# Kernel optimization log

Hardware: AMD Instinct MI355X
Metric: run time of the kernel (lower is better)

Reference implementation:

```python
import jax, jax.numpy as jnp
import numpy as np

D, H, K = 384, 6, 8
B, NQ, NK = 4, 2048, 2048
EPS = 1e-5


def _ln(x, s, b):
    m = jnp.mean(x, axis=-1, keepdims=True)
    v = jnp.mean((x - m) ** 2, axis=-1, keepdims=True)
    return (x - m) * jax.lax.rsqrt(v + EPS) * s + b


def _mha(q, k, v, Wo, bo):
    # q,k,v: [B, N, D]
    dh = D // H
    qh = q.reshape(q.shape[0], q.shape[1], H, dh).transpose(0, 2, 1, 3)
    kh = k.reshape(k.shape[0], k.shape[1], H, dh).transpose(0, 2, 1, 3)
    vh = v.reshape(v.shape[0], v.shape[1], H, dh).transpose(0, 2, 1, 3)
    scores = jnp.einsum('bhqd,bhkd->bhqk', qh, kh) / jnp.sqrt(jnp.asarray(dh, q.dtype))
    attn = jax.nn.softmax(scores, axis=-1)
    out = jnp.einsum('bhqk,bhkd->bhqd', attn, vh)
    out = out.transpose(0, 2, 1, 3).reshape(q.shape[0], q.shape[1], D)
    return out @ Wo + bo


def _knn_edge(q_coords, k_coords, q_feats, k_feats):
    # coords: [B, N, 3]; feats: [B, N, D]. EdgeConv-style feature:
    # concat(neighbor_feat - center_feat, center_feat) -> [B, Nq, K, 2D]
    d2 = (jnp.sum(q_coords ** 2, -1)[:, :, None]
          + jnp.sum(k_coords ** 2, -1)[:, None, :]
          - 2.0 * jnp.einsum('bqc,bkc->bqk', q_coords, k_coords))
    _, idx = jax.lax.top_k(-d2, K)  # [B, Nq, K] nearest neighbors in key set
    neigh = jax.vmap(lambda f, i: f[i])(k_feats, idx)  # [B, Nq, K, D]
    center = jnp.broadcast_to(q_feats[:, :, None, :], neigh.shape)
    return jnp.concatenate([neigh - center, center], axis=-1)


def setup_inputs() -> dict:
    key = jax.random.key(0)
    ks = jax.random.split(key, 24)
    s = 0.02
    return {
        'query_points': jax.random.normal(ks[0], (B, 3 + D, NQ), jnp.float32),
        'key_points': jax.random.normal(ks[1], (B, 3 + D, NK), jnp.float32),
        'ln_in_s': jnp.ones((D,), jnp.float32), 'ln_in_b': jnp.zeros((D,), jnp.float32),
        'qkv_W': jax.random.normal(ks[2], (D, 3 * D), jnp.float32) * s,
        'attn_out_W': jax.random.normal(ks[3], (D, D), jnp.float32) * s,
        'attn_out_b': jnp.zeros((D,), jnp.float32),
        'ff_W1': jax.random.normal(ks[4], (D, 2 * D), jnp.float32) * s,
        'ff_b1': jnp.zeros((2 * D,), jnp.float32),
        'ff_W2': jax.random.normal(ks[5], (2 * D, D), jnp.float32) * s,
        'ff_b2': jnp.zeros((D,), jnp.float32),
        'ffn_s': jnp.ones((D,), jnp.float32), 'ffn_b': jnp.zeros((D,), jnp.float32),
        'knn1_W': jax.random.normal(ks[6], (2 * D, D), jnp.float32) * s,
        'knn1_b': jnp.zeros((D,), jnp.float32),
        'knn2_W': jax.random.normal(ks[7], (2 * D, D), jnp.float32) * s,
        'knn2_b': jnp.zeros((D,), jnp.float32),
        'self_merge_W': jax.random.normal(ks[8], (2 * D, D), jnp.float32) * s,
        'self_merge_b': jnp.zeros((D,), jnp.float32),
        'cross_merge_W': jax.random.normal(ks[9], (2 * D, D), jnp.float32) * s,
        'cross_merge_b': jnp.zeros((D,), jnp.float32),
        'cnq_s': jnp.ones((D,), jnp.float32), 'cnq_b': jnp.zeros((D,), jnp.float32),
        'cnk_s': jnp.ones((D,), jnp.float32), 'cnk_b': jnp.zeros((D,), jnp.float32),
        'cq_W': jax.random.normal(ks[10], (D, D), jnp.float32) * s,
        'ck_W': jax.random.normal(ks[11], (D, D), jnp.float32) * s,
        'cv_W': jax.random.normal(ks[12], (D, D), jnp.float32) * s,
    }


def reference(query_points, key_points, ln_in_s, ln_in_b, qkv_W, attn_out_W,
              attn_out_b, ff_W1, ff_b1, ff_W2, ff_b2, ffn_s, ffn_b,
              knn1_W, knn1_b, knn2_W, knn2_b, self_merge_W, self_merge_b,
              cross_merge_W, cross_merge_b, cnq_s, cnq_b, cnk_s, cnk_b,
              cq_W, ck_W, cv_W):
    qp = jnp.transpose(query_points, (0, 2, 1))  # [B, Nq, 3+D]
    kp = jnp.transpose(key_points, (0, 2, 1))    # [B, Nk, 3+D]
    q_coords, q_feats = qp[..., :3], qp[..., 3:]
    k_coords, k_feats = kp[..., :3], kp[..., 3:]

    # --- self attention + self kNN geometry ---
    norm_f = _ln(q_feats, ln_in_s, ln_in_b)
    qkv = norm_f @ qkv_W
    q, k, v = jnp.split(qkv, 3, axis=-1)
    attn_f = _mha(q, k, v, attn_out_W, attn_out_b)

    edge = _knn_edge(q_coords, q_coords, norm_f, norm_f)          # [B,Nq,K,2D]
    geom = jax.nn.leaky_relu(edge @ knn1_W + knn1_b, 0.2)
    geom = jnp.max(geom, axis=2)                                   # [B,Nq,D]

    attn_f = jnp.concatenate([attn_f, geom], axis=-1) @ self_merge_W + self_merge_b
    q_feats = attn_f + q_feats

    # --- cross attention + cross kNN geometry ---
    nq = _ln(q_feats, cnq_s, cnq_b)
    nk = _ln(k_feats, cnk_s, cnk_b)
    cross_f = _mha(nq @ cq_W, nk @ ck_W, nk @ cv_W, attn_out_W, attn_out_b)

    cedge = _knn_edge(q_coords, k_coords, nq, nk)                  # [B,Nq,K,2D]
    cgeom = jax.nn.leaky_relu(cedge @ knn2_W + knn2_b, 0.2)
    cgeom = jnp.max(cgeom, axis=2)

    cross_f = jnp.concatenate([cross_f, cgeom], axis=-1) @ cross_merge_W + cross_merge_b
    q_feats = q_feats + cross_f

    # --- feed forward ---
    h = _ln(q_feats, ffn_s, ffn_b)
    q_feats = q_feats + (jax.nn.gelu(h @ ff_W1 + ff_b1) @ ff_W2 + ff_b2)

    out = jnp.concatenate([q_coords, q_feats], axis=-1)
    return jnp.transpose(out, (0, 2, 1))  # [B, 3+D, Nq]
```

## Files before the change

kernel.cpp:

```cpp
#include <hip/hip_runtime.h>
#include <cstdint>
#include <cstddef>

#define NB 4
#define NN 2048
#define DD 384
#define NH 6

typedef float f4 __attribute__((ext_vector_type(4)));
typedef float f32x4 __attribute__((ext_vector_type(4)));
typedef short bf16x8 __attribute__((ext_vector_type(8)));
typedef unsigned u32x2 __attribute__((ext_vector_type(2)));

__device__ __forceinline__ float gelu_t(float x) {
  float x3 = x*x*x;
  return 0.5f*x*(1.0f + tanhf(0.7978845608028654f*(x + 0.044715f*x3)));
}

__device__ __forceinline__ unsigned short f2b(float f) {
  unsigned u = __builtin_bit_cast(unsigned, f);
  u += 0x7fffu + ((u >> 16) & 1u);
  return (unsigned short)(u >> 16);
}

__device__ __forceinline__ float b2f(unsigned short u) {
  return __builtin_bit_cast(float, ((unsigned)u) << 16);
}

__device__ __forceinline__ unsigned cvtpk(float a, float b) {
  unsigned r;
  asm("v_cvt_pk_bf16_f32 %0, %1, %2" : "=v"(r) : "v"(a), "v"(b));
  return r;
}

typedef __attribute__((address_space(1))) const void gvoid_t;
typedef __attribute__((address_space(3))) void lvoid_t;
__device__ __forceinline__ void gl16(const void* g, void* l) {
  __builtin_amdgcn_global_load_lds((gvoid_t*)g, (lvoid_t*)l, 16, 0, 0);
}

__device__ __forceinline__ unsigned long long shfl_xor_u64(unsigned long long v, int m) {
  unsigned lo = (unsigned)v, hi = (unsigned)(v >> 32);
  lo = (unsigned)__shfl_xor((int)lo, m);
  hi = (unsigned)__shfl_xor((int)hi, m);
  return ((unsigned long long)hi << 32) | lo;
}

__global__ __launch_bounds__(256) void split_k(const float* __restrict__ pts,
                                               float* __restrict__ coords,
                                               float* __restrict__ feats) {
  __shared__ float t[32][33];
  int b = blockIdx.z;
  int c0 = blockIdx.x*32, n0 = blockIdx.y*32;
  int tx = threadIdx.x, ty = threadIdx.y;
#pragma unroll
  for (int i = 0; i < 4; ++i) {
    int c = c0 + ty + i*8;
    if (c < 387) t[ty+i*8][tx] = pts[((size_t)b*387 + c)*NN + n0 + tx];
  }
  __syncthreads();
#pragma unroll
  for (int i = 0; i < 4; ++i) {
    int n = n0 + ty + i*8;
    int c = c0 + tx;
    if (c < 387) {
      float v = t[tx][ty+i*8];
      if (c < 3) coords[((size_t)b*NN + n)*4 + c] = v;
      else       feats[((size_t)b*NN + n)*DD + (c-3)] = v;
    }
  }
}

__global__ __launch_bounds__(256) void kprep_k(float* __restrict__ c4) {
  int i = blockIdx.x*256 + threadIdx.x;
  f4 v = *(f4*)(c4 + (size_t)i*4);
  v[3] = v[0]*v[0] + v[1]*v[1] + v[2]*v[2];
  *(f4*)(c4 + (size_t)i*4) = v;
}

__global__ __launch_bounds__(256) void pack_k(const float* __restrict__ coords,
                                              const float* __restrict__ feats,
                                              float* __restrict__ out) {
  __shared__ float t[32][33];
  int b = blockIdx.z;
  int c0 = blockIdx.x*32, n0 = blockIdx.y*32;
  int tx = threadIdx.x, ty = threadIdx.y;
#pragma unroll
  for (int i = 0; i < 4; ++i) {
    int n = n0 + ty + i*8;
    int c = c0 + tx;
    if (c < 387) {
      float v = (c < 3) ? coords[((size_t)b*NN + n)*4 + c]
                        : feats[((size_t)b*NN + n)*DD + (c-3)];
      t[tx][ty+i*8] = v;
    }
  }
  __syncthreads();
#pragma unroll
  for (int i = 0; i < 4; ++i) {
    int c = c0 + ty + i*8;
    if (c < 387) out[((size_t)b*387 + c)*NN + n0 + tx] = t[ty+i*8][tx];
  }
}

__device__ __forceinline__ void ln_body(const float* __restrict__ x,
                                        const float* __restrict__ g,
                                        const float* __restrict__ bb,
                                        unsigned short* __restrict__ o,
                                        int row) {
  int lane = threadIdx.x & 63;
  const float* xr = x + (size_t)row*DD;
  float v[6]; float s = 0.f;
#pragma unroll
  for (int i = 0; i < 6; ++i) { v[i] = xr[lane + i*64]; s += v[i]; }
#pragma unroll
  for (int off = 1; off < 64; off <<= 1) s += __shfl_xor(s, off);
  float mean = s * (1.f/384.f);
  float s2 = 0.f;
#pragma unroll
  for (int i = 0; i < 6; ++i) { float d = v[i] - mean; s2 += d*d; }
#pragma unroll
  for (int off = 1; off < 64; off <<= 1) s2 += __shfl_xor(s2, off);
  float rs = rsqrtf(s2*(1.f/384.f) + 1e-5f);
  unsigned short* orow = o + (size_t)row*DD;
#pragma unroll
  for (int i = 0; i < 6; ++i) {
    int c = lane + i*64;
    orow[c] = f2b((v[i]-mean)*rs*g[c] + bb[c]);
  }
}

__global__ __launch_bounds__(256) void ln_k(const float* __restrict__ x,
                                            const float* __restrict__ g,
                                            const float* __restrict__ bb,
                                            unsigned short* __restrict__ o) {
  ln_body(x, g, bb, o, blockIdx.x*4 + (threadIdx.x >> 6));
}

__global__ __launch_bounds__(256) void ln2_k(const float* __restrict__ x1,
                                             const float* __restrict__ g1,
                                             const float* __restrict__ b1,
                                             unsigned short* __restrict__ o1,
                                             const float* __restrict__ x2,
                                             const float* __restrict__ g2,
                                             const float* __restrict__ b2,
                                             unsigned short* __restrict__ o2) {
  int row = blockIdx.x*4 + (threadIdx.x >> 6);
  if (blockIdx.y == 0) ln_body(x1, g1, b1, o1, row);
  else                 ln_body(x2, g2, b2, o2, row);
}

struct WSrcs { const float* p[13]; };

__global__ __launch_bounds__(256) void wtrans_k(WSrcs srcs, unsigned short* __restrict__ dst) {
  constexpr int KK[13]  = {384,384,384,384,768,384,384,384,384,384,768,384,768};
  constexpr int NW[13]  = {1152,384,384,384,384,384,384,384,384,384,384,768,384};
  constexpr int MD[13]  = {0,0,2,0,0,0,0,0,0,2,0,0,0};
  constexpr int OFF[13] = {0,442368,589824,737280,884736,1179648,1327104,1474560,
                           1622016,1769472,1916928,2211840,2506752};
  constexpr int PFX[14] = {0,432,576,720,864,1152,1296,1440,1584,1728,1872,2160,2448,2736};
  int bid = blockIdx.x;
  int e = 0;
  while (bid >= PFX[e+1]) ++e;
  int t = bid - PFX[e];
  int K = KK[e], N = NW[e];
  int ntiles = N >> 5;
  int kt = t / ntiles, nt = t - kt*ntiles;
  const float* src = srcs.p[e];
  __shared__ float T[32][33];
  int tx = threadIdx.x & 31, ty = threadIdx.x >> 5;
  int n = nt*32 + tx;
#pragma unroll
  for (int i = 0; i < 4; ++i) {
    int k = kt*32 + ty + i*8;
    float v = src[(size_t)k*N + n];
    if (MD[e] == 2) v = src[(size_t)(k+384)*N + n] - v;
    T[ty+i*8][tx] = v;
  }
  __syncthreads();
#pragma unroll
  for (int i = 0; i < 4; ++i) {
    int nn = nt*32 + ty + i*8;
    int kk = kt*32 + tx;
    dst[(size_t)OFF[e] + (size_t)nn*K + kk] = f2b(T[tx][ty+i*8]);
  }
}

template<int ACT, int ACC, int OB>
__global__ __launch_bounds__(256) void mgemm_k(const unsigned short* __restrict__ A, int lda,
                                               const unsigned short* __restrict__ Wt,
                                               const float* __restrict__ bias,
                                               void* __restrict__ Cv, int ldc, int cofs,
                                               int Kd) {
  __shared__ char lds[49152];
  int tid = threadIdx.x;
  int lane = tid & 63, w = tid >> 6, g = lane >> 4, c = lane & 15;
  int wr = w >> 1, wc = w & 1;
  int m0 = blockIdx.y*128, n0 = blockIdx.x*64;
  int lrow = lane >> 3;
  int cswz = ((lane & 7) ^ lrow)*8;

  f32x4 acc[4][2];
#pragma unroll
  for (int mt = 0; mt < 4; ++mt)
#pragma unroll
    for (int nt = 0; nt < 2; ++nt) acc[mt][nt] = 0.f;

  int KT = Kd >> 6;
  {
    char* As = lds; char* Bs = lds + 16384;
#pragma unroll
    for (int i = 0; i < 4; ++i) {
      int rb = i*32 + w*8;
      gl16(A + (size_t)(m0 + rb + lrow)*lda + cswz, As + rb*128);
    }
#pragma unroll
    for (int i = 0; i < 2; ++i) {
      int rb = i*32 + w*8;
      gl16(Wt + (size_t)(n0 + rb + lrow)*Kd + cswz, Bs + rb*128);
    }
  }
  __syncthreads();

  for (int kt = 0; kt < KT; ++kt) {
    char* Asc = lds + (kt & 1)*24576;
    char* Bsc = Asc + 16384;
    if (kt + 1 < KT) {
      char* Asn = lds + ((kt + 1) & 1)*24576;
      char* Bsn = Asn + 16384;
      int k0 = (kt + 1)*64;
#pragma unroll
      for (int i = 0; i < 4; ++i) {
        int rb = i*32 + w*8;
        gl16(A + (size_t)(m0 + rb + lrow)*lda + k0 + cswz, Asn + rb*128);
      }
#pragma unroll
      for (int i = 0; i < 2; ++i) {
        int rb = i*32 + w*8;
        gl16(Wt + (size_t)(n0 + rb + lrow)*Kd + k0 + cswz, Bsn + rb*128);
      }
    }
#pragma unroll
    for (int kb = 0; kb < 2; ++kb) {
      bf16x8 af[4], bfr[2];
#pragma unroll
      for (int mt = 0; mt < 4; ++mt) {
        int row = wr*64 + mt*16 + c;
        int ch = (kb*4 + g) ^ (row & 7);
        af[mt] = *(const bf16x8*)(Asc + row*128 + ch*16);
      }
#pragma unroll
      for (int nt = 0; nt < 2; ++nt) {
        int row = wc*32 + nt*16 + c;
        int ch = (kb*4 + g) ^ (row & 7);
        bfr[nt] = *(const bf16x8*)(Bsc + row*128 + ch*16);
      }
#pragma unroll
      for (int mt = 0; mt < 4; ++mt)
#pragma unroll
        for (int nt = 0; nt < 2; ++nt)
          acc[mt][nt] = __builtin_amdgcn_mfma_f32_16x16x32_bf16(af[mt], bfr[nt], acc[mt][nt], 0, 0, 0);
    }
    __syncthreads();
  }

#pragma unroll
  for (int mt = 0; mt < 4; ++mt) {
#pragma unroll
    for (int nt = 0; nt < 2; ++nt) {
      int coln = n0 + wc*32 + nt*16 + c;
      float bval = bias ? bias[coln] : 0.f;
#pragma unroll
      for (int r = 0; r < 4; ++r) {
        int m = m0 + wr*64 + mt*16 + 4*g + r;
        float t = acc[mt][nt][r] + bval;
        if (ACT == 1) t = gelu_t(t);
        if (OB) {
          ((unsigned short*)Cv)[(size_t)m*ldc + cofs + coln] = f2b(t);
        } else {
          float* cp = (float*)Cv + (size_t)m*ldc + cofs + coln;
          if (ACC) t += *cp;
          *cp = t;
        }
      }
    }
  }
}

struct FSegs {
  const unsigned short* A[5];
  unsigned short* out[5];
  int ldc[5];
  int cofs[5];
};

__global__ __launch_bounds__(256) void fgemm_k(FSegs fs, const unsigned short* __restrict__ Wt) {
  __shared__ char lds[49152];
  int tid = threadIdx.x;
  int lane = tid & 63, w = tid >> 6, g = lane >> 4, c = lane & 15;
  int wr = w >> 1, wc = w & 1;
  int m0 = blockIdx.y*128, n0 = blockIdx.x*64;
  int seg = n0 / 384;
  const unsigned short* A = fs.A[seg];
  int lrow = lane >> 3;
  int cswz = ((lane & 7) ^ lrow)*8;

  f32x4 acc[4][2];
#pragma unroll
  for (int mt = 0; mt < 4; ++mt)
#pragma unroll
    for (int nt = 0; nt < 2; ++nt) acc[mt][nt] = 0.f;

  {
    char* As = lds; char* Bs = lds + 16384;
#pragma unroll
    for (int i = 0; i < 4; ++i) {
      int rb = i*32 + w*8;
      gl16(A + (size_t)(m0 + rb + lrow)*384 + cswz, As + rb*128);
    }
#pragma unroll
    for (int i = 0; i < 2; ++i) {
      int rb = i*32 + w*8;
      gl16(Wt + (size_t)(n0 + rb + lrow)*384 + cswz, Bs + rb*128);
    }
  }
  __syncthreads();

  for (int kt = 0; kt < 6; ++kt) {
    char* Asc = lds + (kt & 1)*24576;
    char* Bsc = Asc + 16384;
    if (kt + 1 < 6) {
      char* Asn = lds + ((kt + 1) & 1)*24576;
      char* Bsn = Asn + 16384;
      int k0 = (kt + 1)*64;
#pragma unroll
      for (int i = 0; i < 4; ++i) {
        int rb = i*32 + w*8;
        gl16(A + (size_t)(m0 + rb + lrow)*384 + k0 + cswz, Asn + rb*128);
      }
#pragma unroll
      for (int i = 0; i < 2; ++i) {
        int rb = i*32 + w*8;
        gl16(Wt + (size_t)(n0 + rb + lrow)*384 + k0 + cswz, Bsn + rb*128);
      }
    }
#pragma unroll
    for (int kb = 0; kb < 2; ++kb) {
      bf16x8 af[4], bfr[2];
#pragma unroll
      for (int mt = 0; mt < 4; ++mt) {
        int row = wr*64 + mt*16 + c;
        int ch = (kb*4 + g) ^ (row & 7);
        af[mt] = *(const bf16x8*)(Asc + row*128 + ch*16);
      }
#pragma unroll
      for (int nt = 0; nt < 2; ++nt) {
        int row = wc*32 + nt*16 + c;
        int ch = (kb*4 + g) ^ (row & 7);
        bfr[nt] = *(const bf16x8*)(Bsc + row*128 + ch*16);
      }
#pragma unroll
      for (int mt = 0; mt < 4; ++mt)
#pragma unroll
        for (int nt = 0; nt < 2; ++nt)
          acc[mt][nt] = __builtin_amdgcn_mfma_f32_16x16x32_bf16(af[mt], bfr[nt], acc[mt][nt], 0, 0, 0);
    }
    __syncthreads();
  }

  if (seg == 2) {
    unsigned short* vtp = fs.out[2];
    int bb = m0 >> 11;
    int tokb = (m0 & 2047) + wr*64 + 4*g;
#pragma unroll
    for (int mt = 0; mt < 4; ++mt) {
#pragma unroll
      for (int nt = 0; nt < 2; ++nt) {
        int cseg = (n0 - 768) + wc*32 + nt*16 + c;
        int h = cseg >> 6, d = cseg & 63;
        u32x2 pv;
        pv[0] = cvtpk(acc[mt][nt][0], acc[mt][nt][1]);
        pv[1] = cvtpk(acc[mt][nt][2], acc[mt][nt][3]);
        *(u32x2*)(vtp + ((size_t)((bb*NH + h)*64 + d))*NN + tokb + mt*16) = pv;
      }
    }
    return;
  }

  unsigned short* outp = fs.out[seg];
  int ldcs = fs.ldc[seg];
  int cbase = fs.cofs[seg] + (n0 - seg*384);
#pragma unroll
  for (int mt = 0; mt < 4; ++mt) {
#pragma unroll
    for (int nt = 0; nt < 2; ++nt) {
      int coln = cbase + wc*32 + nt*16 + c;
#pragma unroll
      for (int r = 0; r < 4; ++r) {
        int m = m0 + wr*64 + mt*16 + 4*g + r;
        outp[(size_t)m*ldcs + coln] = f2b(acc[mt][nt][r]);
      }
    }
  }
}

__global__ __launch_bounds__(256) void flashm_k(const unsigned short* __restrict__ qkvb,
                                                const unsigned short* __restrict__ vt,
                                                unsigned short* __restrict__ o) {
  __shared__ char smem[40960];
  char* PT = smem + 32768;
  int bid = blockIdx.x;
  int s = (bid & 7)*96 + (bid >> 3);
  int qt = s & 31; int hb = s >> 5;
  int h = hb % NH, b = hb / NH;
  int q0 = qt*64;
  int tid = threadIdx.x;
  int w = tid >> 6, lane = tid & 63, g = lane >> 4, c = lane & 15;
  int lrow = lane >> 3;
  int gsw = ((lane & 7) ^ lrow)*8;

  const unsigned short* kbase = qkvb + (size_t)b*NN*1152 + 384 + h*64;
  const unsigned short* vbase = vt + ((size_t)(b*NH + h))*64*NN;

  bf16x8 qf[2];
  {
    const unsigned short* qrow = qkvb + ((size_t)(b*NN + q0 + w*16 + c))*1152 + h*64;
    qf[0] = *(const bf16x8*)(qrow + 8*g);
    qf[1] = *(const bf16x8*)(qrow + 32 + 8*g);
  }
  f32x4 oacc[4];
#pragma unroll
  for (int i = 0; i < 4; ++i) oacc[i] = 0.f;
  float lsum = 0.f;

#define FSTAGE(bf, ktb) { \
    char* KB = smem + (bf)*16384; char* VB = KB + 8192; \
    gl16(kbase + (size_t)((ktb) + w*16 + lrow)*1152 + gsw,     KB + (w*16)*128); \
    gl16(kbase + (size_t)((ktb) + w*16 + 8 + lrow)*1152 + gsw, KB + (w*16+8)*128); \
    gl16(vbase + (size_t)(w*16 + lrow)*NN + (ktb) + gsw,       VB + (w*16)*128); \
    gl16(vbase + (size_t)(w*16 + 8 + lrow)*NN + (ktb) + gsw,   VB + (w*16+8)*128); }

  FSTAGE(0, 0);
  __syncthreads();

  for (int kt = 0; kt < 32; ++kt) {
    if (kt + 1 < 32) FSTAGE((kt + 1) & 1, (kt + 1)*64);
    char* KTc = smem + (kt & 1)*16384;
    char* VTc = KTc + 8192;

    f32x4 sT[4];
#pragma unroll
    for (int nt = 0; nt < 4; ++nt) sT[nt] = 0.f;
#pragma unroll
    for (int nt = 0; nt < 4; ++nt) {
      int krow = nt*16 + c;
#pragma unroll
      for (int kb = 0; kb < 2; ++kb) {
        int ch = ((kb*4 + g) ^ (krow & 7))*16;
        bf16x8 kf_ = *(const bf16x8*)(KTc + krow*128 + ch);
        sT[nt] = __builtin_amdgcn_mfma_f32_16x16x32_bf16(kf_, qf[kb], sT[nt], 0, 0, 0);
      }
    }

    int prow = w*16 + c;
    int pswz = (c & 7) << 4;
#pragma unroll
    for (int nt = 0; nt < 4; ++nt) {
      float p0 = __builtin_amdgcn_exp2f(sT[nt][0] * 0.18033688011112042f);
      float p1 = __builtin_amdgcn_exp2f(sT[nt][1] * 0.18033688011112042f);
      float p2 = __builtin_amdgcn_exp2f(sT[nt][2] * 0.18033688011112042f);
      float p3 = __builtin_amdgcn_exp2f(sT[nt][3] * 0.18033688011112042f);
      lsum += (p0 + p1) + (p2 + p3);
      u32x2 pk;
      pk[0] = cvtpk(p0, p1);
      pk[1] = cvtpk(p2, p3);
      *(u32x2*)(PT + prow*128 + ((nt*32 + 8*g) ^ pswz)) = pk;
    }

    bf16x8 pb[2];
#pragma unroll
    for (int kb = 0; kb < 2; ++kb)
      pb[kb] = *(const bf16x8*)(PT + prow*128 + (((kb*4 + g) ^ (c & 7))*16));

#pragma unroll
    for (int dt = 0; dt < 4; ++dt) {
      int vrow = dt*16 + c;
#pragma unroll
      for (int kb = 0; kb < 2; ++kb) {
        int ch = ((kb*4 + g) ^ (vrow & 7))*16;
        bf16x8 vf = *(const bf16x8*)(VTc + vrow*128 + ch);
        oacc[dt] = __builtin_amdgcn_mfma_f32_16x16x32_bf16(vf, pb[kb], oacc[dt], 0, 0, 0);
      }
    }
    __syncthreads();
  }
#undef FSTAGE

  lsum += __shfl_xor(lsum, 16);
  lsum += __shfl_xor(lsum, 32);
  float inv = 1.f / lsum;
  size_t orow = ((size_t)b*NN + q0 + w*16 + c)*DD + h*64;
#pragma unroll
  for (int dt = 0; dt < 4; ++dt) {
    u32x2 ov;
    ov[0] = cvtpk(oacc[dt][0]*inv, oacc[dt][1]*inv);
    ov[1] = cvtpk(oacc[dt][2]*inv, oacc[dt][3]*inv);
    *(u32x2*)(o + orow + dt*16 + 4*g) = ov;
  }
}

#define CEX(a, b) { \
  unsigned long long lo_ = bd[a] < bd[b] ? bd[a] : bd[b]; \
  unsigned long long hi_ = bd[a] < bd[b] ? bd[b] : bd[a]; \
  bd[a] = lo_; bd[b] = hi_; }

__global__ __launch_bounds__(256) void knn2_k(const float* __restrict__ qc4,
                                              const float* __restrict__ kc4,
                                              int* __restrict__ idx1,
                                              int* __restrict__ idx2) {
  const float* kcs = blockIdx.y ? kc4 : qc4;
  int* idxo = blockIdx.y ? idx2 : idx1;
  int lane = threadIdx.x & 63;
  int q = blockIdx.x*4 + (threadIdx.x >> 6);
  int b = q >> 11;
  f4 qv = *(const f4*)(qc4 + (size_t)q*4);
  unsigned long long bd[8];
#pragma unroll
  for (int i = 0; i < 8; ++i) bd[i] = ~0ull;
  const float* kb = kcs + (size_t)b*NN*4;
#pragma unroll 4
  for (int j = lane; j < NN; j += 64) {
    f4 kv = *(const f4*)(kb + (size_t)j*4);
    float f = kv[3] - 2.f*(qv[0]*kv[0] + qv[1]*kv[1] + qv[2]*kv[2]);
    unsigned u = __builtin_bit_cast(unsigned, f);
    u ^= 0x80000000u | (unsigned)((int)u >> 31);
    unsigned long long key = ((unsigned long long)u << 32) | (unsigned)j;
#pragma unroll
    for (int k = 0; k < 8; ++k) {
      unsigned long long lo = key < bd[k] ? key : bd[k];
      unsigned long long hi = key < bd[k] ? bd[k] : key;
      bd[k] = lo; key = hi;
    }
  }
#pragma unroll
  for (int m = 1; m <= 32; m <<= 1) {
    unsigned long long pr[8];
#pragma unroll
    for (int i = 0; i < 8; ++i) pr[i] = shfl_xor_u64(bd[7-i], m);
#pragma unroll
    for (int i = 0; i < 8; ++i) bd[i] = bd[i] < pr[i] ? bd[i] : pr[i];
    CEX(0,4) CEX(1,5) CEX(2,6) CEX(3,7)
    CEX(0,2) CEX(1,3) CEX(4,6) CEX(5,7)
    CEX(0,1) CEX(2,3) CEX(4,5) CEX(6,7)
  }
  if (lane == 0) {
#pragma unroll
    for (int r = 0; r < 8; ++r) idxo[(size_t)q*8 + r] = (int)(unsigned)bd[r];
  }
}

__global__ __launch_bounds__(384) void geom_k(const unsigned short* __restrict__ GCb,
                                              const float* __restrict__ bias,
                                              const int* __restrict__ idx,
                                              unsigned short* __restrict__ out) {
  int q = blockIdx.x;
  int b = q >> 11;
  int d = threadIdx.x;
  float c = b2f(GCb[(size_t)q*768 + 384 + d]) + bias[d];
  float mx = -INFINITY;
#pragma unroll
  for (int kn = 0; kn < 8; ++kn) {
    int j = idx[(size_t)q*8 + kn];
    float gg = b2f(GCb[((size_t)(b << 11) + j)*768 + d]);
    float y = gg + c;
    y = (y > 0.f) ? y : 0.2f*y;
    mx = fmaxf(mx, y);
  }
  out[(size_t)q*768 + 384 + d] = f2b(mx);
}

extern "C" void kernel_launch(void* const* d_in, const int* in_sizes, int n_in,
                              void* d_out, int out_size, void* d_ws, size_t ws_size,
                              hipStream_t stream) {
  (void)in_sizes; (void)n_in; (void)out_size; (void)ws_size;
  const float* qpts  = (const float*)d_in[0];
  const float* kpts  = (const float*)d_in[1];
  const float* ln_s  = (const float*)d_in[2];
  const float* ln_b  = (const float*)d_in[3];
  const float* qkvW  = (const float*)d_in[4];
  const float* Wo    = (const float*)d_in[5];
  const float* bo    = (const float*)d_in[6];
  const float* ffW1  = (const float*)d_in[7];
  const float* ffb1  = (const float*)d_in[8];
  const float* ffW2  = (const float*)d_in[9];
  const float* ffb2  = (const float*)d_in[10];
  const float* ffns  = (const float*)d_in[11];
  const float* ffnb  = (const float*)d_in[12];
  const float* knn1W = (const float*)d_in[13];
  const float* knn1b = (const float*)d_in[14];
  const float* knn2W = (const float*)d_in[15];
  const float* knn2b = (const float*)d_in[16];
  const float* smW   = (const float*)d_in[17];
  const float* smb   = (const float*)d_in[18];
  const float* cmW   = (const float*)d_in[19];
  const float* cmb   = (const float*)d_in[20];
  const float* cnqs  = (const float*)d_in[21];
  const float* cnqb  = (const float*)d_in[22];
  const float* cnks  = (const float*)d_in[23];
  const float* cnkb  = (const float*)d_in[24];
  const float* cqW   = (const float*)d_in[25];
  const float* ckW   = (const float*)d_in[26];
  const float* cvW   = (const float*)d_in[27];

  float* ws = (float*)d_ws;
  float* qc4  = ws;
  float* kc4  = qc4 + 32768;
  float* qf   = kc4 + 32768;
  float* kf   = qf + 3145728;
  unsigned short* nrmb = (unsigned short*)(kf + 3145728);
  unsigned short* nkb  = (unsigned short*)(kf + 3145728 + 1572864);
  float* qkv = kf + 3145728 + 1572864 + 1572864;
  unsigned short* qkvb   = (unsigned short*)qkv;
  unsigned short* attnGb = (unsigned short*)qkv;
  unsigned short* vtb    = (unsigned short*)(qkv + 4718592);
  unsigned short* wtb    = (unsigned short*)(qkv + 4718592 + 1572864);
  unsigned short* attnOb = (unsigned short*)(qkv + 4718592 + 1572864 + 1400832);
  unsigned short* GCbb   = (unsigned short*)((float*)attnOb + 1572864);
  int* idx1 = (int*)((float*)GCbb + 3145728);
  int* idx2 = idx1 + 65536;

  const int W_FA=0, W_WO=737280, W_SM=884736, W_FB=1179648,
            W_CM=1916928, W_FF1=2211840, W_FF2=2506752;

  WSrcs srcs;
  srcs.p[0]=qkvW; srcs.p[1]=knn1W; srcs.p[2]=knn1W; srcs.p[3]=Wo; srcs.p[4]=smW;
  srcs.p[5]=cqW; srcs.p[6]=ckW; srcs.p[7]=cvW; srcs.p[8]=knn2W; srcs.p[9]=knn2W;
  srcs.p[10]=cmW; srcs.p[11]=ffW1; srcs.p[12]=ffW2;
  wtrans_k<<<2736, 256, 0, stream>>>(srcs, wtb);

  dim3 tgrid(13, 64, NB), tblk(32, 8);
  split_k<<<tgrid, tblk, 0, stream>>>(qpts, qc4, qf);
  split_k<<<tgrid, tblk, 0, stream>>>(kpts, kc4, kf);
  kprep_k<<<64, 256, 0, stream>>>(qc4);

  knn2_k<<<dim3(2048, 2), 256, 0, stream>>>(qc4, kc4, idx1, idx2);

  dim3 mg384(6, 64), mg768(12, 64), fg(30, 64);

  ln_k<<<2048, 256, 0, stream>>>(qf, ln_s, ln_b, nrmb);
  {
    FSegs fa;
    for (int s = 0; s < 5; ++s) fa.A[s] = nrmb;
    fa.out[0] = qkvb; fa.ldc[0] = 1152; fa.cofs[0] = 0;
    fa.out[1] = qkvb; fa.ldc[1] = 1152; fa.cofs[1] = 384;
    fa.out[2] = vtb;  fa.ldc[2] = 0;    fa.cofs[2] = 0;
    fa.out[3] = GCbb; fa.ldc[3] = 768;  fa.cofs[3] = 0;
    fa.out[4] = GCbb; fa.ldc[4] = 768;  fa.cofs[4] = 384;
    fgemm_k<<<fg, 256, 0, stream>>>(fa, wtb + W_FA);
  }
  flashm_k<<<768, 256, 0, stream>>>(qkvb, vtb, attnOb);
  mgemm_k<0,0,1><<<mg384, 256, 0, stream>>>(attnOb, DD, wtb+W_WO, bo, attnGb, 768, 0, DD);
  geom_k<<<8192, 384, 0, stream>>>(GCbb, knn1b, idx1, attnGb);
  mgemm_k<0,1,0><<<mg384, 256, 0, stream>>>(attnGb, 768, wtb+W_SM, smb, qf, DD, 0, 768);

  ln2_k<<<dim3(2048, 2), 256, 0, stream>>>(qf, cnqs, cnqb, nrmb, kf, cnks, cnkb, nkb);
  {
    FSegs fb;
    fb.A[0] = nrmb; fb.A[1] = nkb; fb.A[2] = nkb; fb.A[3] = nkb; fb.A[4] = nrmb;
    fb.out[0] = qkvb; fb.ldc[0] = 1152; fb.cofs[0] = 0;
    fb.out[1] = qkvb; fb.ldc[1] = 1152; fb.cofs[1] = 384;
    fb.out[2] = vtb;  fb.ldc[2] = 0;    fb.cofs[2] = 0;
    fb.out[3] = GCbb; fb.ldc[3] = 768;  fb.cofs[3] = 0;
    fb.out[4] = GCbb; fb.ldc[4] = 768;  fb.cofs[4] = 384;
    fgemm_k<<<fg, 256, 0, stream>>>(fb, wtb + W_FB);
  }
  flashm_k<<<768, 256, 0, stream>>>(qkvb, vtb, attnOb);
  mgemm_k<0,0,1><<<mg384, 256, 0, stream>>>(attnOb, DD, wtb+W_WO, bo, attnGb, 768, 0, DD);
  geom_k<<<8192, 384, 0, stream>>>(GCbb, knn2b, idx2, attnGb);
  mgemm_k<0,1,0><<<mg384, 256, 0, stream>>>(attnGb, 768, wtb+W_CM, cmb, qf, DD, 0, 768);

  ln_k<<<2048, 256, 0, stream>>>(qf, ffns, ffnb, nrmb);
  mgemm_k<1,0,1><<<mg768, 256, 0, stream>>>(nrmb, DD, wtb+W_FF1, ffb1, attnGb, 768, 0, DD);
  mgemm_k<0,1,0><<<mg384, 256, 0, stream>>>(attnGb, 768, wtb+W_FF2, ffb2, qf, DD, 0, 768);

  pack_k<<<tgrid, tblk, 0, stream>>>(qc4, qf, (float*)d_out);
}
```

Before: 379.6 us.

## Add two-pass threshold kNN and half-height GEMM tiles for N=384 GEMMs

The kNN kernel now runs a cheap float-only top-8 pass over register-cached distances to find the 8th-smallest threshold, then inserts only candidates at or below it into the 64-bit key/index sorted list, guarded by a wave-wide any vote. This targets the costly 64-bit compare-swap chain per candidate. Separately, the GEMM kernel gains a HALFM variant with 64-row tiles, used for the 384-wide output GEMMs so they launch twice as many blocks. That should fill the GPU better, at the cost of less reuse of each weight tile and more register pressure from the 32 cached distances in kNN.

```diff
diff --git a/kernel.cpp b/kernel.cpp
--- a/kernel.cpp
+++ b/kernel.cpp
@@ -186,31 +186,36 @@
   }
 }
 
-template<int ACT, int ACC, int OB>
+template<int ACT, int ACC, int OB, int HALFM>
 __global__ __launch_bounds__(256) void mgemm_k(const unsigned short* __restrict__ A, int lda,
                                                const unsigned short* __restrict__ Wt,
                                                const float* __restrict__ bias,
                                                void* __restrict__ Cv, int ldc, int cofs,
                                                int Kd) {
-  __shared__ char lds[49152];
+  constexpr int BM   = HALFM ? 64 : 128;
+  constexpr int MT   = HALFM ? 2 : 4;
+  constexpr int AG   = HALFM ? 2 : 4;
+  constexpr int ABUF = BM*128;
+  constexpr int BUFSZ = ABUF + 8192;
+  __shared__ char lds[2*BUFSZ];
   int tid = threadIdx.x;
   int lane = tid & 63, w = tid >> 6, g = lane >> 4, c = lane & 15;
   int wr = w >> 1, wc = w & 1;
-  int m0 = blockIdx.y*128, n0 = blockIdx.x*64;
+  int m0 = blockIdx.y*BM, n0 = blockIdx.x*64;
   int lrow = lane >> 3;
   int cswz = ((lane & 7) ^ lrow)*8;
 
-  f32x4 acc[4][2];
-#pragma unroll
-  for (int mt = 0; mt < 4; ++mt)
+  f32x4 acc[MT][2];
+#pragma unroll
+  for (int mt = 0; mt < MT; ++mt)
 #pragma unroll
     for (int nt = 0; nt < 2; ++nt) acc[mt][nt] = 0.f;
 
   int KT = Kd >> 6;
   {
-    char* As = lds; char* Bs = lds + 16384;
-#pragma unroll
-    for (int i = 0; i < 4; ++i) {
+    char* As = lds; char* Bs = lds + ABUF;
+#pragma unroll
+    for (int i = 0; i < AG; ++i) {
       int rb = i*32 + w*8;
       gl16(A + (size_t)(m0 + rb + lrow)*lda + cswz, As + rb*128);
     }
@@ -223,14 +228,14 @@
   __syncthreads();
 
   for (int kt = 0; kt < KT; ++kt) {
-    char* Asc = lds + (kt & 1)*24576;
-    char* Bsc = Asc + 16384;
+    char* Asc = lds + (kt & 1)*BUFSZ;
+    char* Bsc = Asc + ABUF;
     if (kt + 1 < KT) {
-      char* Asn = lds + ((kt + 1) & 1)*24576;
-      char* Bsn = Asn + 16384;
+      char* Asn = lds + ((kt + 1) & 1)*BUFSZ;
+      char* Bsn = Asn + ABUF;
       int k0 = (kt + 1)*64;
 #pragma unroll
-      for (int i = 0; i < 4; ++i) {
+      for (int i = 0; i < AG; ++i) {
         int rb = i*32 + w*8;
         gl16(A + (size_t)(m0 + rb + lrow)*lda + k0 + cswz, Asn + rb*128);
       }
@@ -242,10 +247,10 @@
     }
 #pragma unroll
     for (int kb = 0; kb < 2; ++kb) {
-      bf16x8 af[4], bfr[2];
-#pragma unroll
-      for (int mt = 0; mt < 4; ++mt) {
-        int row = wr*64 + mt*16 + c;
+      bf16x8 af[MT], bfr[2];
+#pragma unroll
+      for (int mt = 0; mt < MT; ++mt) {
+        int row = wr*(BM/2) + mt*16 + c;
         int ch = (kb*4 + g) ^ (row & 7);
         af[mt] = *(const bf16x8*)(Asc + row*128 + ch*16);
       }
@@ -256,7 +261,7 @@
         bfr[nt] = *(const bf16x8*)(Bsc + row*128 + ch*16);
       }
 #pragma unroll
-      for (int mt = 0; mt < 4; ++mt)
+      for (int mt = 0; mt < MT; ++mt)
 #pragma unroll
         for (int nt = 0; nt < 2; ++nt)
           acc[mt][nt] = __builtin_amdgcn_mfma_f32_16x16x32_bf16(af[mt], bfr[nt], acc[mt][nt], 0, 0, 0);
@@ -265,14 +270,14 @@
   }
 
 #pragma unroll
-  for (int mt = 0; mt < 4; ++mt) {
+  for (int mt = 0; mt < MT; ++mt) {
 #pragma unroll
     for (int nt = 0; nt < 2; ++nt) {
       int coln = n0 + wc*32 + nt*16 + c;
       float bval = bias ? bias[coln] : 0.f;
 #pragma unroll
       for (int r = 0; r < 4; ++r) {
-        int m = m0 + wr*64 + mt*16 + 4*g + r;
+        int m = m0 + wr*(BM/2) + mt*16 + 4*g + r;
         float t = acc[mt][nt][r] + bval;
         if (ACT == 1) t = gelu_t(t);
         if (OB) {
@@ -509,6 +514,11 @@
   }
 }
 
+#define CEXF(a, b) { \
+  float lo_ = fminf(bf[a], bf[b]); \
+  float hi_ = fmaxf(bf[a], bf[b]); \
+  bf[a] = lo_; bf[b] = hi_; }
+
 #define CEX(a, b) { \
   unsigned long long lo_ = bd[a] < bd[b] ? bd[a] : bd[b]; \
   unsigned long long hi_ = bd[a] < bd[b] ? bd[b] : bd[a]; \
@@ -524,22 +534,53 @@
   int q = blockIdx.x*4 + (threadIdx.x >> 6);
   int b = q >> 11;
   f4 qv = *(const f4*)(qc4 + (size_t)q*4);
+  float mx_ = -2.f*qv[0], my_ = -2.f*qv[1], mz_ = -2.f*qv[2];
+  const float* kb = kcs + (size_t)b*NN*4;
+
+  float fv[32];
+  float bf[8];
+#pragma unroll
+  for (int i = 0; i < 8; ++i) bf[i] = INFINITY;
+#pragma unroll
+  for (int i = 0; i < 32; ++i) {
+    f4 kv = *(const f4*)(kb + (size_t)(lane + i*64)*4);
+    float f = fmaf(mx_, kv[0], fmaf(my_, kv[1], fmaf(mz_, kv[2], kv[3])));
+    fv[i] = f;
+#pragma unroll
+    for (int k = 0; k < 8; ++k) {
+      float lo = fminf(f, bf[k]);
+      float hi = fmaxf(f, bf[k]);
+      bf[k] = lo; f = hi;
+    }
+  }
+#pragma unroll
+  for (int m = 1; m <= 32; m <<= 1) {
+    float pr[8];
+#pragma unroll
+    for (int i = 0; i < 8; ++i) pr[i] = __shfl_xor(bf[7-i], m);
+#pragma unroll
+    for (int i = 0; i < 8; ++i) bf[i] = fminf(bf[i], pr[i]);
+    CEXF(0,4) CEXF(1,5) CEXF(2,6) CEXF(3,7)
+    CEXF(0,2) CEXF(1,3) CEXF(4,6) CEXF(5,7)
+    CEXF(0,1) CEXF(2,3) CEXF(4,5) CEXF(6,7)
+  }
+  float T = bf[7];
+
   unsigned long long bd[8];
 #pragma unroll
   for (int i = 0; i < 8; ++i) bd[i] = ~0ull;
-  const float* kb = kcs + (size_t)b*NN*4;
-#pragma unroll 4
-  for (int j = lane; j < NN; j += 64) {
-    f4 kv = *(const f4*)(kb + (size_t)j*4);
-    float f = kv[3] - 2.f*(qv[0]*kv[0] + qv[1]*kv[1] + qv[2]*kv[2]);
-    unsigned u = __builtin_bit_cast(unsigned, f);
-    u ^= 0x80000000u | (unsigned)((int)u >> 31);
-    unsigned long long key = ((unsigned long long)u << 32) | (unsigned)j;
-#pragma unroll
-    for (int k = 0; k < 8; ++k) {
-      unsigned long long lo = key < bd[k] ? key : bd[k];
-      unsigned long long hi = key < bd[k] ? bd[k] : key;
-      bd[k] = lo; key = hi;
+#pragma unroll
+  for (int i = 0; i < 32; ++i) {
+    if (__any(fv[i] <= T)) {
+      unsigned u = __builtin_bit_cast(unsigned, fv[i]);
+      u ^= 0x80000000u | (unsigned)((int)u >> 31);
+      unsigned long long key = ((unsigned long long)u << 32) | (unsigned)(lane + i*64);
+#pragma unroll
+      for (int k = 0; k < 8; ++k) {
+        unsigned long long lo = key < bd[k] ? key : bd[k];
+        unsigned long long hi = key < bd[k] ? bd[k] : key;
+        bd[k] = lo; key = hi;
+      }
     }
   }
 #pragma unroll
@@ -645,7 +686,7 @@
 
   knn2_k<<<dim3(2048, 2), 256, 0, stream>>>(qc4, kc4, idx1, idx2);
 
-  dim3 mg384(6, 64), mg768(12, 64), fg(30, 64);
+  dim3 mg384h(6, 128), mg768(12, 64), fg(30, 64);
 
   ln_k<<<2048, 256, 0, stream>>>(qf, ln_s, ln_b, nrmb);
   {
@@ -659,9 +700,9 @@
     fgemm_k<<<fg, 256, 0, stream>>>(fa, wtb + W_FA);
   }
   flashm_k<<<768, 256, 0, stream>>>(qkvb, vtb, attnOb);
-  mgemm_k<0,0,1><<<mg384, 256, 0, stream>>>(attnOb, DD, wtb+W_WO, bo, attnGb, 768, 0, DD);
+  mgemm_k<0,0,1,1><<<mg384h, 256, 0, stream>>>(attnOb, DD, wtb+W_WO, bo, attnGb, 768, 0, DD);
   geom_k<<<8192, 384, 0, stream>>>(GCbb, knn1b, idx1, attnGb);
-  mgemm_k<0,1,0><<<mg384, 256, 0, stream>>>(attnGb, 768, wtb+W_SM, smb, qf, DD, 0, 768);
+  mgemm_k<0,1,0,1><<<mg384h, 256, 0, stream>>>(attnGb, 768, wtb+W_SM, smb, qf, DD, 0, 768);
 
   ln2_k<<<dim3(2048, 2), 256, 0, stream>>>(qf, cnqs, cnqb, nrmb, kf, cnks, cnkb, nkb);
   {
@@ -675,13 +716,13 @@
     fgemm_k<<<fg, 256, 0, stream>>>(fb, wtb + W_FB);
   }
   flashm_k<<<768, 256, 0, stream>>>(qkvb, vtb, attnOb);
-  mgemm_k<0,0,1><<<mg384, 256, 0, stream>>>(attnOb, DD, wtb+W_WO, bo, attnGb, 768, 0, DD);
+  mgemm_k<0,0,1,1><<<mg384h, 256, 0, stream>>>(attnOb, DD, wtb+W_WO, bo, attnGb, 768, 0, DD);
   geom_k<<<8192, 384, 0, stream>>>(GCbb, knn2b, idx2, attnGb);
-  mgemm_k<0,1,0><<<mg384, 256, 0, stream>>>(attnGb, 768, wtb+W_CM, cmb, qf, DD, 0, 768);
+  mgemm_k<0,1,0,1><<<mg384h, 256, 0, stream>>>(attnGb, 768, wtb+W_CM, cmb, qf, DD, 0, 768);
 
   ln_k<<<2048, 256, 0, stream>>>(qf, ffns, ffnb, nrmb);
-  mgemm_k<1,0,1><<<mg768, 256, 0, stream>>>(nrmb, DD, wtb+W_FF1, ffb1, attnGb, 768, 0, DD);
-  mgemm_k<0,1,0><<<mg384, 256, 0, stream>>>(attnGb, 768, wtb+W_FF2, ffb2, qf, DD, 0, 768);
+  mgemm_k<1,0,1,0><<<mg768, 256, 0, stream>>>(nrmb, DD, wtb+W_FF1, ffb1, attnGb, 768, 0, DD);
+  mgemm_k<0,1,0,1><<<mg384h, 256, 0, stream>>>(attnGb, 768, wtb+W_FF2, ffb2, qf, DD, 0, 768);
 
   pack_k<<<tgrid, tblk, 0, stream>>>(qc4, qf, (float*)d_out);
 }
```

After: 352.1 us. 7.3% less time.
